# Optimization experiments

Hardware: AMD Instinct MI355X
Metric: run time of the kernel (lower is better)

Reference implementation:

```python
import jax, jax.numpy as jnp
import numpy as np

B = 2048        # batch of independent trajectories
N = 10000       # number of time points (N-1 Euler steps)
H = 64          # hidden width of the augmentation MLP
DT = 0.001


def _mlp(z, W1, b1, W2, b2, W3, b3):
    # z: (B, 2) -> (B, 1) damping correction (replaces -mu*(1-z0^2)*z1 term)
    h = jnp.tanh(z @ W1 + b1)
    h = jnp.tanh(h @ W2 + b2)
    return h @ W3 + b3


def setup_inputs() -> dict:
    key = jax.random.key(0)
    k0, k1, k2, k3 = jax.random.split(key, 4)
    z0 = jax.random.normal(k0, (B, 2), dtype=jnp.float32)
    t = (jnp.arange(N, dtype=jnp.float32) * DT)
    ode_params = jnp.array([3.0, 5.0, 1.0], dtype=jnp.float32)  # kappa, mu, mass
    W1 = jax.random.normal(k1, (2, H), dtype=jnp.float32) * (1.0 / np.sqrt(2))
    b1 = jnp.zeros((H,), dtype=jnp.float32)
    W2 = jax.random.normal(k2, (H, H), dtype=jnp.float32) * (1.0 / np.sqrt(H))
    b2 = jnp.zeros((H,), dtype=jnp.float32)
    W3 = jax.random.normal(k3, (H, 1), dtype=jnp.float32) * (1.0 / np.sqrt(H))
    b3 = jnp.zeros((1,), dtype=jnp.float32)
    return {"z0": z0, "t": t, "ode_params": ode_params,
            "W1": W1, "b1": b1, "W2": W2, "b2": b2, "W3": W3, "b3": b3}


def reference(z0, t, ode_params, W1, b1, W2, b2, W3, b3):
    """Forward-Euler integration of the hybrid ODE (fused scan, no stim).

    dz0/dt = z1
    dz1/dt = -kappa * z0 / mass + NN(z)
    Returns trajectory of shape (N, B, 2); row 0 is z0 (matches z[0]=z0).
    """
    kappa = ode_params[0]
    mass = ode_params[2]
    dts = t[1:] - t[:-1]  # (N-1,)

    def step(z, dt):
        nn_out = _mlp(z, W1, b1, W2, b2, W3, b3)[:, 0]          # (B,)
        dz = jnp.stack([z[:, 1], -kappa * z[:, 0] / mass + nn_out], axis=-1)
        z_next = z + dt * dz
        return z_next, z_next

    _, traj = jax.lax.scan(step, z0, dts)                        # (N-1, B, 2)
    return jnp.concatenate([z0[None], traj], axis=0)             # (N, B, 2)
```

## Files before the change

kernel.cpp:

```cpp
#include <hip/hip_runtime.h>

#define NB 2048
#define NT 10000

typedef __fp16 half2_t __attribute__((ext_vector_type(2)));
typedef __fp16 half8_t __attribute__((ext_vector_type(8)));
typedef float  float4_t __attribute__((ext_vector_type(4)));

template <int CTRL>
__device__ __forceinline__ float dpp_f(float x) {
    return __int_as_float(__builtin_amdgcn_mov_dpp(__float_as_int(x), CTRL, 0xF, 0xF, true));
}
#define DPP_XOR1 0xB1
#define DPP_XOR2 0x4E
#define DPP_HMIR 0x141
#define DPP_MIR  0x140
#define DPP_BC15 0x142
#define DPP_BC31 0x143

__device__ __forceinline__ float readlane_f(float v, int l) {
    return __int_as_float(__builtin_amdgcn_readlane(__float_as_int(v), l));
}

__device__ __forceinline__ float fast_tanh_from_scaled(float pre_scaled) {
    float e = __builtin_amdgcn_exp2f(pre_scaled);
    return fmaf(-2.0f, __builtin_amdgcn_rcpf(1.0f + e), 1.0f);
}

__global__ __launch_bounds__(64, 2) void hybrid_euler_kernel(
    const float* __restrict__ z0in,
    const float* __restrict__ t,
    const float* __restrict__ prm,
    const float* __restrict__ W1,
    const float* __restrict__ b1,
    const float* __restrict__ W2,
    const float* __restrict__ b2,
    const float* __restrict__ W3,
    const float* __restrict__ b3,
    float* __restrict__ out)
{
    const int lane = threadIdx.x;
    const int b    = blockIdx.x;
    const int m    = lane & 15;
    const int kg   = lane >> 4;

    const float S = 2.8853900817779268f;

    const float w1a = W1[lane]      * S;
    const float w1b = W1[64 + lane] * S;
    const float b1v = b1[lane]      * S;

    half8_t w2f[4][2];
    #pragma unroll
    for (int tile = 0; tile < 4; ++tile) {
        const int col = tile * 16 + m;
        #pragma unroll
        for (int h = 0; h < 2; ++h) {
            half8_t f;
            #pragma unroll
            for (int e = 0; e < 8; ++e) {
                const int k = h * 32 + kg * 8 + e;
                f[e] = (__fp16)(W2[k * 64 + col] * S);
            }
            w2f[tile][h] = f;
        }
    }

    float4_t cb[4];
    #pragma unroll
    for (int tile = 0; tile < 4; ++tile) {
        const float v = b2[tile * 16 + m] * S;
        float4_t q;
        q[0] = v; q[1] = v; q[2] = v; q[3] = v;
        cb[tile] = q;
    }

    const float w3v   = W3[lane];
    const float b3_64 = b3[0] * 0.015625f;
    const float kappa = prm[0];
    const float mass  = prm[2];
    const float kmoM  = -kappa / mass;

    __shared__ alignas(16) int hbuf[64];

    float z0 = z0in[b * 2 + 0];
    float z1 = z0in[b * 2 + 1];

    if (lane == 0) {
        *(float2*)(out + (size_t)b * 2) = make_float2(z0, z1);
    }

    const int widx = (lane >> 1) + ((lane & 1) << 5);
    const bool kb0 = (lane & 16) != 0;
    const bool kb1 = (lane & 32) != 0;

    float tprev = t[0];
    float tcur  = t[1];
    float* optr = out + (size_t)NB * 2 + (size_t)b * 2;

    for (int s = 1; s < NT; ++s) {
        const float tnext = (s + 1 < NT) ? t[s + 1] : tcur;
        const float dt = tcur - tprev;

        const float pre1 = fmaf(z0, w1a, fmaf(z1, w1b, b1v));
        const float h1 = fast_tanh_from_scaled(pre1);

        const float h1n = dpp_f<DPP_XOR1>(h1);
        const int hpi = __builtin_bit_cast(int,
            __builtin_amdgcn_cvt_pkrtz(h1, h1n));

        hbuf[widx] = hpi;
        asm volatile("" ::: "memory");
        half8_t a0, a1;
        __builtin_memcpy(&a0, &hbuf[kg * 4],      16);
        __builtin_memcpy(&a1, &hbuf[16 + kg * 4], 16);

        float4_t acc[4];
        #pragma unroll
        for (int tile = 0; tile < 4; ++tile) {
            acc[tile] = __builtin_amdgcn_mfma_f32_16x16x32_f16(
                a1, w2f[tile][1],
                __builtin_amdgcn_mfma_f32_16x16x32_f16(a0, w2f[tile][0], cb[tile], 0, 0, 0),
                0, 0, 0);
        }

        const float a01 = kb0 ? acc[1][0] : acc[0][0];
        const float a23 = kb0 ? acc[3][0] : acc[2][0];
        const float pre2 = kb1 ? a23 : a01;
        const float h2 = fast_tanh_from_scaled(pre2);
        float p = fmaf(h2, w3v, b3_64);

        p += dpp_f<DPP_XOR1>(p);
        p += dpp_f<DPP_XOR2>(p);
        p += dpp_f<DPP_HMIR>(p);
        p += dpp_f<DPP_MIR>(p);
        p += dpp_f<DPP_BC15>(p);
        p += dpp_f<DPP_BC31>(p);
        const float nn = readlane_f(p, 63);

        const float z1n = fmaf(dt, fmaf(kmoM, z0, nn), z1);
        const float z0n = fmaf(dt, z1, z0);
        z0 = z0n; z1 = z1n;

        if (lane == 0) {
            *(float2*)optr = make_float2(z0, z1);
        }
        optr += (size_t)NB * 2;

        tprev = tcur;
        tcur  = tnext;
    }
}

extern "C" void kernel_launch(void* const* d_in, const int* in_sizes, int n_in,
                              void* d_out, int out_size, void* d_ws, size_t ws_size,
                              hipStream_t stream) {
    const float* z0 = (const float*)d_in[0];
    const float* t  = (const float*)d_in[1];
    const float* pp = (const float*)d_in[2];
    const float* W1 = (const float*)d_in[3];
    const float* b1 = (const float*)d_in[4];
    const float* W2 = (const float*)d_in[5];
    const float* b2 = (const float*)d_in[6];
    const float* W3 = (const float*)d_in[7];
    const float* b3 = (const float*)d_in[8];
    float* out = (float*)d_out;

    hybrid_euler_kernel<<<dim3(NB), dim3(64), 0, stream>>>(
        z0, t, pp, W1, b1, W2, b2, W3, b3, out);
}
```

Measured before the change: 2.600 ms.

## Process two trajectories per wavefront to interleave independent dependency chains

Each 64-lane block now integrates two trajectories instead of one and the grid is halved to 1024 blocks. The two independent MLP evaluations per step (tanh, DPP transposes, MFMAs, reductions) are interleaved, so one chain can hide the latency of the other within a single wave. Outputs for both trajectories are written with one float4 store, and launch bounds drop to one wave per EU minimum. The cost is higher register pressure and fewer waves available to the scheduler.

```diff
diff --git a/kernel.cpp b/kernel.cpp
--- a/kernel.cpp
+++ b/kernel.cpp
@@ -2,6 +2,7 @@
 
 #define NB 2048
 #define NT 10000
+#define NBLK 1024
 
 typedef __fp16 half2_t __attribute__((ext_vector_type(2)));
 typedef __fp16 half8_t __attribute__((ext_vector_type(8)));
@@ -27,7 +28,7 @@
     return fmaf(-2.0f, __builtin_amdgcn_rcpf(1.0f + e), 1.0f);
 }
 
-__global__ __launch_bounds__(64, 2) void hybrid_euler_kernel(
+__global__ __launch_bounds__(64, 1) void hybrid_euler_kernel(
     const float* __restrict__ z0in,
     const float* __restrict__ t,
     const float* __restrict__ prm,
@@ -40,7 +41,7 @@
     float* __restrict__ out)
 {
     const int lane = threadIdx.x;
-    const int b    = blockIdx.x;
+    const int bp   = blockIdx.x;
     const int m    = lane & 15;
     const int kg   = lane >> 4;
 
@@ -81,13 +82,13 @@
     const float mass  = prm[2];
     const float kmoM  = -kappa / mass;
 
-    __shared__ alignas(16) int hbuf[64];
+    __shared__ alignas(16) int hbuf[128];
 
-    float z0 = z0in[b * 2 + 0];
-    float z1 = z0in[b * 2 + 1];
+    const float4 zi = *(const float4*)(z0in + bp * 4);
+    float zA0 = zi.x, zA1 = zi.y, zB0 = zi.z, zB1 = zi.w;
 
     if (lane == 0) {
-        *(float2*)(out + (size_t)b * 2) = make_float2(z0, z1);
+        *(float4*)(out + (size_t)bp * 4) = zi;
     }
 
     const int widx = (lane >> 1) + ((lane & 1) << 5);
@@ -96,54 +97,73 @@
 
     float tprev = t[0];
     float tcur  = t[1];
-    float* optr = out + (size_t)NB * 2 + (size_t)b * 2;
+    float* optr = out + (size_t)NB * 2 + (size_t)bp * 4;
 
     for (int s = 1; s < NT; ++s) {
         const float tnext = (s + 1 < NT) ? t[s + 1] : tcur;
         const float dt = tcur - tprev;
 
-        const float pre1 = fmaf(z0, w1a, fmaf(z1, w1b, b1v));
-        const float h1 = fast_tanh_from_scaled(pre1);
+        const float pre1A = fmaf(zA0, w1a, fmaf(zA1, w1b, b1v));
+        const float pre1B = fmaf(zB0, w1a, fmaf(zB1, w1b, b1v));
+        const float h1A = fast_tanh_from_scaled(pre1A);
+        const float h1B = fast_tanh_from_scaled(pre1B);
 
-        const float h1n = dpp_f<DPP_XOR1>(h1);
-        const int hpi = __builtin_bit_cast(int,
-            __builtin_amdgcn_cvt_pkrtz(h1, h1n));
+        const float h1An = dpp_f<DPP_XOR1>(h1A);
+        const float h1Bn = dpp_f<DPP_XOR1>(h1B);
+        const int hpiA = __builtin_bit_cast(int, __builtin_amdgcn_cvt_pkrtz(h1A, h1An));
+        const int hpiB = __builtin_bit_cast(int, __builtin_amdgcn_cvt_pkrtz(h1B, h1Bn));
 
-        hbuf[widx] = hpi;
+        hbuf[widx]      = hpiA;
+        hbuf[64 + widx] = hpiB;
         asm volatile("" ::: "memory");
-        half8_t a0, a1;
-        __builtin_memcpy(&a0, &hbuf[kg * 4],      16);
-        __builtin_memcpy(&a1, &hbuf[16 + kg * 4], 16);
+        half8_t a0A, a1A, a0B, a1B;
+        __builtin_memcpy(&a0A, &hbuf[kg * 4],           16);
+        __builtin_memcpy(&a1A, &hbuf[16 + kg * 4],      16);
+        __builtin_memcpy(&a0B, &hbuf[64 + kg * 4],      16);
+        __builtin_memcpy(&a1B, &hbuf[64 + 16 + kg * 4], 16);
 
-        float4_t acc[4];
+        float4_t accA[4], accB[4];
         #pragma unroll
         for (int tile = 0; tile < 4; ++tile) {
-            acc[tile] = __builtin_amdgcn_mfma_f32_16x16x32_f16(
-                a1, w2f[tile][1],
-                __builtin_amdgcn_mfma_f32_16x16x32_f16(a0, w2f[tile][0], cb[tile], 0, 0, 0),
+            accA[tile] = __builtin_amdgcn_mfma_f32_16x16x32_f16(
+                a1A, w2f[tile][1],
+                __builtin_amdgcn_mfma_f32_16x16x32_f16(a0A, w2f[tile][0], cb[tile], 0, 0, 0),
+                0, 0, 0);
+            accB[tile] = __builtin_amdgcn_mfma_f32_16x16x32_f16(
+                a1B, w2f[tile][1],
+                __builtin_amdgcn_mfma_f32_16x16x32_f16(a0B, w2f[tile][0], cb[tile], 0, 0, 0),
                 0, 0, 0);
         }
 
-        const float a01 = kb0 ? acc[1][0] : acc[0][0];
-        const float a23 = kb0 ? acc[3][0] : acc[2][0];
-        const float pre2 = kb1 ? a23 : a01;
-        const float h2 = fast_tanh_from_scaled(pre2);
-        float p = fmaf(h2, w3v, b3_64);
+        const float a01A = kb0 ? accA[1][0] : accA[0][0];
+        const float a23A = kb0 ? accA[3][0] : accA[2][0];
+        const float a01B = kb0 ? accB[1][0] : accB[0][0];
+        const float a23B = kb0 ? accB[3][0] : accB[2][0];
+        const float pre2A = kb1 ? a23A : a01A;
+        const float pre2B = kb1 ? a23B : a01B;
+        const float h2A = fast_tanh_from_scaled(pre2A);
+        const float h2B = fast_tanh_from_scaled(pre2B);
+        float pA = fmaf(h2A, w3v, b3_64);
+        float pB = fmaf(h2B, w3v, b3_64);
 
-        p += dpp_f<DPP_XOR1>(p);
-        p += dpp_f<DPP_XOR2>(p);
-        p += dpp_f<DPP_HMIR>(p);
-        p += dpp_f<DPP_MIR>(p);
-        p += dpp_f<DPP_BC15>(p);
-        p += dpp_f<DPP_BC31>(p);
-        const float nn = readlane_f(p, 63);
+        pA += dpp_f<DPP_XOR1>(pA);  pB += dpp_f<DPP_XOR1>(pB);
+        pA += dpp_f<DPP_XOR2>(pA);  pB += dpp_f<DPP_XOR2>(pB);
+        pA += dpp_f<DPP_HMIR>(pA);  pB += dpp_f<DPP_HMIR>(pB);
+        pA += dpp_f<DPP_MIR>(pA);   pB += dpp_f<DPP_MIR>(pB);
+        pA += dpp_f<DPP_BC15>(pA);  pB += dpp_f<DPP_BC15>(pB);
+        pA += dpp_f<DPP_BC31>(pA);  pB += dpp_f<DPP_BC31>(pB);
+        const float nnA = readlane_f(pA, 63);
+        const float nnB = readlane_f(pB, 63);
 
-        const float z1n = fmaf(dt, fmaf(kmoM, z0, nn), z1);
-        const float z0n = fmaf(dt, z1, z0);
-        z0 = z0n; z1 = z1n;
+        const float zA1n = fmaf(dt, fmaf(kmoM, zA0, nnA), zA1);
+        const float zA0n = fmaf(dt, zA1, zA0);
+        const float zB1n = fmaf(dt, fmaf(kmoM, zB0, nnB), zB1);
+        const float zB0n = fmaf(dt, zB1, zB0);
+        zA0 = zA0n; zA1 = zA1n; zB0 = zB0n; zB1 = zB1n;
 
         if (lane == 0) {
-            *(float2*)optr = make_float2(z0, z1);
+            float4 st; st.x = zA0; st.y = zA1; st.z = zB0; st.w = zB1;
+            *(float4*)optr = st;
         }
         optr += (size_t)NB * 2;
 
@@ -166,6 +186,6 @@
     const float* b3 = (const float*)d_in[8];
     float* out = (float*)d_out;
 
-    hybrid_euler_kernel<<<dim3(NB), dim3(64), 0, stream>>>(
+    hybrid_euler_kernel<<<dim3(NBLK), dim3(64), 0, stream>>>(
         z0, t, pp, W1, b1, W2, b2, W3, b3, out);
 }
```

New measurement: 3.842 ms. 47.8% more time.
